# Kernel tuning notes

Measured on AMD Instinct MI355X. Metric: run time of the kernel, lower is better.

## Reference

```python
import jax, jax.numpy as jnp
import numpy as np
import math

S = 30.0
M = 0.5
COS_M = math.cos(M)
SIN_M = math.sin(M)
TH = math.cos(math.pi - M)  # threshold cos(pi - m)
EPS = 1e-12  # matches F.normalize default eps


def setup_inputs() -> dict:
    key = jax.random.key(0)
    k1, k2, k3 = jax.random.split(key, 3)
    B, D, C = 1024, 512, 100000
    inp = jax.random.normal(k1, (B, D), dtype=jnp.float32)
    label = jax.random.randint(k2, (B,), 0, C)
    # xavier_uniform_ for weight of shape (C, D): bound = sqrt(6/(C+D))
    bound = math.sqrt(6.0 / (C + D))
    weight = jax.random.uniform(k3, (C, D), dtype=jnp.float32, minval=-bound, maxval=bound)
    return {"input": inp, "label": label, "weight": weight}


def _l2norm(x):
    # F.normalize: x / max(||x||, eps)
    n = jnp.sqrt(jnp.sum(x * x, axis=-1, keepdims=True))
    return x / jnp.maximum(n, EPS)


def reference(input, label, weight):
    # cosine: [B, C]
    cosine = jnp.einsum('bd,cd->bc', _l2norm(input), _l2norm(weight))
    sine = jnp.sqrt(jnp.clip(1.0 - cosine * cosine, 0.0, 1.0))
    phi = cosine * COS_M - sine * SIN_M
    phi = jnp.where(cosine > TH, phi, cosine - S * SIN_M * M)
    # one-hot combine done via direct label-indexed select (avoids materializing one_hot)
    B, C = cosine.shape
    is_target = jnp.arange(C)[None, :] == label[:, None]  # [B, C] bool
    output = jnp.where(is_target, phi, cosine) * S
    return output
```

## Files before the change

### kernel.cpp

```cpp
#include <hip/hip_runtime.h>


#define MDIM 1024
#define KDIM 512
#define NCLS 100000

#define BM 128
#define BN 128
#define BK 32
#define LDST 40

#define NTILES ((NCLS + BN - 1) / BN)
#define NWG (8 * NTILES)

typedef unsigned short u16;
typedef unsigned int u32;
typedef short s16x8 __attribute__((ext_vector_type(8)));
typedef float f32x4 __attribute__((ext_vector_type(4)));

__device__ __forceinline__ u32 pk2(float a, float b) {
  u32 ua = __builtin_bit_cast(u32, a);
  u32 ub = __builtin_bit_cast(u32, b);
  ua += 0x7FFFu + ((ua >> 16) & 1u);
  ub += 0x7FFFu + ((ub >> 16) & 1u);
  return (ua >> 16) | (ub & 0xFFFF0000u);
}

__global__ __launch_bounds__(256) void norm_input_kernel(const float* __restrict__ in,
                                                         u16* __restrict__ abf) {
  const int row = blockIdx.x;
  const int tid = threadIdx.x;
  const float2 v = *reinterpret_cast<const float2*>(in + (size_t)row * KDIM + 2 * tid);
  float ss = v.x * v.x + v.y * v.y;
#pragma unroll
  for (int off = 32; off > 0; off >>= 1) ss += __shfl_down(ss, off);
  __shared__ float part[4];
  if ((tid & 63) == 0) part[tid >> 6] = ss;
  __syncthreads();
  const float tot = part[0] + part[1] + part[2] + part[3];
  const float rn = 1.0f / fmaxf(sqrtf(tot), 1e-12f);
  reinterpret_cast<u32*>(abf)[row * (KDIM / 2) + tid] = pk2(v.x * rn, v.y * rn);
}

__global__ __launch_bounds__(256) void norm_weight_kernel(const float* __restrict__ W,
                                                          u16* __restrict__ wbf) {
  const int row = blockIdx.x * 4 + (threadIdx.x >> 6);
  const int lane = threadIdx.x & 63;
  const float* p = W + (size_t)row * KDIM + lane * 8;
  const float4 v0 = *reinterpret_cast<const float4*>(p);
  const float4 v1 = *reinterpret_cast<const float4*>(p + 4);
  float ss = v0.x * v0.x + v0.y * v0.y + v0.z * v0.z + v0.w * v0.w
           + v1.x * v1.x + v1.y * v1.y + v1.z * v1.z + v1.w * v1.w;
#pragma unroll
  for (int off = 32; off > 0; off >>= 1) ss += __shfl_xor(ss, off);
  const float rn = 1.0f / fmaxf(sqrtf(ss), 1e-12f);
  uint4 o;
  o.x = pk2(v0.x * rn, v0.y * rn);
  o.y = pk2(v0.z * rn, v0.w * rn);
  o.z = pk2(v1.x * rn, v1.y * rn);
  o.w = pk2(v1.z * rn, v1.w * rn);
  *reinterpret_cast<uint4*>(wbf + (size_t)row * KDIM + lane * 8) = o;
}

__global__ __launch_bounds__(256) void arcface_gemm_bf16(const u16* __restrict__ Abf,
                                                         const u16* __restrict__ Wbf,
                                                         const int* __restrict__ label,
                                                         float* __restrict__ out) {
  __shared__ u16 lA[BM * LDST];
  __shared__ u16 lW[BN * LDST];
  __shared__ int lbl[BM];

  const int tid = threadIdx.x;
  const int orig = blockIdx.x;
  const int wg = (orig & 7) * NTILES + (orig >> 3);
  const int m0 = (wg & 7) * BM;
  const int n0 = (wg >> 3) * BN;

  if (tid < BM) lbl[tid] = label[m0 + tid];

  const int r = tid >> 1;
  const int half = tid & 1;
  int c = n0 + r;
  if (c >= NCLS) c = NCLS - 1;

  const u16* aptr = Abf + (size_t)(m0 + r) * KDIM + half * 16;
  const u16* wptr = Wbf + (size_t)c * KDIM + half * 16;

  uint4 a0 = *(const uint4*)(aptr);
  uint4 a1 = *(const uint4*)(aptr + 8);
  uint4 b0 = *(const uint4*)(wptr);
  uint4 b1 = *(const uint4*)(wptr + 8);

  f32x4 acc[4][4] = {};

  const int lane = tid & 63;
  const int wv = tid >> 6;
  const int wm = (wv & 1) * 64;
  const int wn = (wv >> 1) * 64;
  const int ln = lane & 15;
  const int kq = lane >> 4;

  const int aw = r * LDST + half * 16;

  for (int kt = 0; kt < KDIM / BK; ++kt) {
    __syncthreads();
    *(uint4*)&lA[aw] = a0;
    *(uint4*)&lA[aw + 8] = a1;
    *(uint4*)&lW[aw] = b0;
    *(uint4*)&lW[aw + 8] = b1;
    __syncthreads();

    if (kt < KDIM / BK - 1) {
      const u16* ap = aptr + (kt + 1) * BK;
      a0 = *(const uint4*)(ap);
      a1 = *(const uint4*)(ap + 8);
      const u16* wp = wptr + (kt + 1) * BK;
      b0 = *(const uint4*)(wp);
      b1 = *(const uint4*)(wp + 8);
    }

    s16x8 af[4], wf[4];
#pragma unroll
    for (int i = 0; i < 4; ++i)
      af[i] = *(const s16x8*)&lA[(wm + 16 * i + ln) * LDST + kq * 8];
#pragma unroll
    for (int j = 0; j < 4; ++j)
      wf[j] = *(const s16x8*)&lW[(wn + 16 * j + ln) * LDST + kq * 8];
#pragma unroll
    for (int i = 0; i < 4; ++i)
#pragma unroll
      for (int j = 0; j < 4; ++j)
        acc[i][j] = __builtin_amdgcn_mfma_f32_16x16x32_bf16(af[i], wf[j], acc[i][j], 0, 0, 0);
  }

  constexpr float S_ = 30.0f;
  constexpr float COS_M = 0.87758256189037276f;
  constexpr float SIN_M = 0.47942553860420301f;
  constexpr float TH_ = -0.87758256189037276f;
  constexpr float FALLB = 30.0f * 0.47942553860420301f * 0.5f;

#pragma unroll
  for (int i = 0; i < 4; ++i) {
    const int lrow_b = wm + 16 * i + 4 * kq;
#pragma unroll
    for (int j = 0; j < 4; ++j) {
      const int col = wn + 16 * j + ln;
      const int gcol = n0 + col;
      if (gcol < NCLS) {
#pragma unroll
        for (int rg = 0; rg < 4; ++rg) {
          const int lrow = lrow_b + rg;
          const float cosv = acc[i][j][rg];
          float o = S_ * cosv;
          if (gcol == lbl[lrow]) {
            const float s2 = fmaxf(1.0f - cosv * cosv, 0.0f);
            const float sine = sqrtf(s2);
            float phi = cosv * COS_M - sine * SIN_M;
            phi = (cosv > TH_) ? phi : (cosv - FALLB);
            o = S_ * phi;
          }
          __builtin_nontemporal_store(o, &out[(size_t)(m0 + lrow) * NCLS + gcol]);
        }
      }
    }
  }
}

__global__ __launch_bounds__(256) void arcface_gemm(const u16* __restrict__ Abf,
                                                    const float* __restrict__ W,
                                                    const int* __restrict__ label,
                                                    float* __restrict__ out) {
  __shared__ u16 lA[BM * LDST];
  __shared__ u16 lW[BN * LDST];
  __shared__ float rnw[BN];
  __shared__ int lbl[BM];

  const int tid = threadIdx.x;
  const int m0 = blockIdx.x * BM;
  const int n0 = blockIdx.y * BN;

  if (tid < BM) lbl[tid] = label[m0 + tid];

  const int r = tid >> 1;
  const int half = tid & 1;
  int c = n0 + r;
  if (c >= NCLS) c = NCLS - 1;

  const u16* aptr = Abf + (size_t)(m0 + r) * KDIM + half * 16;
  const float* wptr = W + (size_t)c * KDIM + half * 16;

  uint4 a0 = *(const uint4*)(aptr);
  uint4 a1 = *(const uint4*)(aptr + 8);
  float4 w0 = *(const float4*)(wptr);
  float4 w1 = *(const float4*)(wptr + 4);
  float4 w2 = *(const float4*)(wptr + 8);
  float4 w3 = *(const float4*)(wptr + 12);

  f32x4 acc[4][4] = {};
  float ss = 0.0f;

  const int lane = tid & 63;
  const int wv = tid >> 6;
  const int wm = (wv & 1) * 64;
  const int wn = (wv >> 1) * 64;
  const int ln = lane & 15;
  const int kq = lane >> 4;

  const int aw = r * LDST + half * 16;

  for (int kt = 0; kt < KDIM / BK; ++kt) {
    __syncthreads();
    *(uint4*)&lA[aw] = a0;
    *(uint4*)&lA[aw + 8] = a1;
    ss += w0.x * w0.x + w0.y * w0.y + w0.z * w0.z + w0.w * w0.w;
    ss += w1.x * w1.x + w1.y * w1.y + w1.z * w1.z + w1.w * w1.w;
    ss += w2.x * w2.x + w2.y * w2.y + w2.z * w2.z + w2.w * w2.w;
    ss += w3.x * w3.x + w3.y * w3.y + w3.z * w3.z + w3.w * w3.w;
    uint4 p0, p1;
    p0.x = pk2(w0.x, w0.y); p0.y = pk2(w0.z, w0.w);
    p0.z = pk2(w1.x, w1.y); p0.w = pk2(w1.z, w1.w);
    p1.x = pk2(w2.x, w2.y); p1.y = pk2(w2.z, w2.w);
    p1.z = pk2(w3.x, w3.y); p1.w = pk2(w3.z, w3.w);
    *(uint4*)&lW[aw] = p0;
    *(uint4*)&lW[aw + 8] = p1;
    __syncthreads();

    if (kt < KDIM / BK - 1) {
      const u16* ap = aptr + (kt + 1) * BK;
      a0 = *(const uint4*)(ap);
      a1 = *(const uint4*)(ap + 8);
      const float* wp = wptr + (kt + 1) * BK;
      w0 = *(const float4*)(wp);
      w1 = *(const float4*)(wp + 4);
      w2 = *(const float4*)(wp + 8);
      w3 = *(const float4*)(wp + 12);
    }

    s16x8 af[4], wf[4];
#pragma unroll
    for (int i = 0; i < 4; ++i)
      af[i] = *(const s16x8*)&lA[(wm + 16 * i + ln) * LDST + kq * 8];
#pragma unroll
    for (int j = 0; j < 4; ++j)
      wf[j] = *(const s16x8*)&lW[(wn + 16 * j + ln) * LDST + kq * 8];
#pragma unroll
    for (int i = 0; i < 4; ++i)
#pragma unroll
      for (int j = 0; j < 4; ++j)
        acc[i][j] = __builtin_amdgcn_mfma_f32_16x16x32_bf16(af[i], wf[j], acc[i][j], 0, 0, 0);
  }

  const float sst = ss + __shfl_xor(ss, 1);
  if (half == 0) rnw[r] = 1.0f / fmaxf(sqrtf(sst), 1e-12f);
  __syncthreads();

  constexpr float S_ = 30.0f;
  constexpr float COS_M = 0.87758256189037276f;
  constexpr float SIN_M = 0.47942553860420301f;
  constexpr float TH_ = -0.87758256189037276f;
  constexpr float FALLB = 30.0f * 0.47942553860420301f * 0.5f;

#pragma unroll
  for (int i = 0; i < 4; ++i) {
    const int lrow_b = wm + 16 * i + 4 * kq;
#pragma unroll
    for (int j = 0; j < 4; ++j) {
      const int col = wn + 16 * j + ln;
      const int gcol = n0 + col;
      const float rw = rnw[col];
      if (gcol < NCLS) {
#pragma unroll
        for (int rg = 0; rg < 4; ++rg) {
          const int lrow = lrow_b + rg;
          const float cosv = acc[i][j][rg] * rw;
          float o = S_ * cosv;
          if (gcol == lbl[lrow]) {
            const float s2 = fmaxf(1.0f - cosv * cosv, 0.0f);
            const float sine = sqrtf(s2);
            float phi = cosv * COS_M - sine * SIN_M;
            phi = (cosv > TH_) ? phi : (cosv - FALLB);
            o = S_ * phi;
          }
          out[(size_t)(m0 + lrow) * NCLS + gcol] = o;
        }
      }
    }
  }
}

extern "C" void kernel_launch(void* const* d_in, const int* in_sizes, int n_in,
                              void* d_out, int out_size, void* d_ws, size_t ws_size,
                              hipStream_t stream) {
  const float* input = (const float*)d_in[0];
  const int* label = (const int*)d_in[1];
  const float* weight = (const float*)d_in[2];
  float* out = (float*)d_out;
  u16* abf = (u16*)d_ws;

  hipLaunchKernelGGL(norm_input_kernel, dim3(MDIM), dim3(256), 0, stream, input, abf);

  const size_t a_bytes = (size_t)MDIM * KDIM * sizeof(u16);
  const size_t w_bytes = (size_t)NCLS * KDIM * sizeof(u16);
  if (ws_size >= a_bytes + w_bytes) {
    u16* wbf = abf + (size_t)MDIM * KDIM;
    hipLaunchKernelGGL(norm_weight_kernel, dim3(NCLS / 4), dim3(256), 0, stream, weight, wbf);
    hipLaunchKernelGGL(arcface_gemm_bf16, dim3(NWG), dim3(256), 0, stream, abf, wbf, label, out);
  } else {
    dim3 grid(MDIM / BM, (NCLS + BN - 1) / BN);
    hipLaunchKernelGGL(arcface_gemm, grid, dim3(256), 0, stream, abf, weight, label, out);
  }
}
```

Measured before the change: 719.2 us.

## Load GEMM tiles directly into LDS with global_load_lds and drop nontemporal stores

Replaces the register-staged global→LDS copy in the bf16 GEMM with direct global_load_lds DMA into a swizzled LDS layout matching MFMA fragment order. Fragments are read into registers before the next tile's async load is issued, which frees VGPRs and removes the explicit LDS write step. The output store also changes from nontemporal to a regular store. This relies on correct waitcnt handling between async LDS loads and the barrier, and the output is write-bound (400MB) so the gain may be limited.

Measured after the change: 785.1 us. 9.2% more time.

```diff
diff --git a/kernel.cpp b/kernel.cpp
--- a/kernel.cpp
+++ b/kernel.cpp
@@ -24,6 +24,12 @@
   ua += 0x7FFFu + ((ua >> 16) & 1u);
   ub += 0x7FFFu + ((ub >> 16) & 1u);
   return (ua >> 16) | (ub & 0xFFFF0000u);
+}
+
+__device__ __forceinline__ void gl16(const u16* g, u16* l) {
+  __builtin_amdgcn_global_load_lds(
+      (const __attribute__((address_space(1))) void*)g,
+      (__attribute__((address_space(3))) void*)l, 16, 0, 0);
 }
 
 __global__ __launch_bounds__(256) void norm_input_kernel(const float* __restrict__ in,
@@ -66,8 +72,8 @@
                                                          const u16* __restrict__ Wbf,
                                                          const int* __restrict__ label,
                                                          float* __restrict__ out) {
-  __shared__ u16 lA[BM * LDST];
-  __shared__ u16 lW[BN * LDST];
+  __shared__ u16 lA[BM * BK];
+  __shared__ u16 lW[BN * BK];
   __shared__ int lbl[BM];
 
   const int tid = threadIdx.x;
@@ -78,54 +84,52 @@
 
   if (tid < BM) lbl[tid] = label[m0 + tid];
 
-  const int r = tid >> 1;
-  const int half = tid & 1;
-  int c = n0 + r;
-  if (c >= NCLS) c = NCLS - 1;
-
-  const u16* aptr = Abf + (size_t)(m0 + r) * KDIM + half * 16;
-  const u16* wptr = Wbf + (size_t)c * KDIM + half * 16;
-
-  uint4 a0 = *(const uint4*)(aptr);
-  uint4 a1 = *(const uint4*)(aptr + 8);
-  uint4 b0 = *(const uint4*)(wptr);
-  uint4 b1 = *(const uint4*)(wptr + 8);
-
-  f32x4 acc[4][4] = {};
-
   const int lane = tid & 63;
   const int wv = tid >> 6;
+
+  const int sr = lane & 15;
+  const int sc = (lane >> 4) * 8;
+  const u16* aG0 = Abf + (size_t)(m0 + 16 * wv + sr) * KDIM + sc;
+  const u16* aG1 = aG0 + (size_t)64 * KDIM;
+  int wr0 = n0 + 16 * wv + sr;       if (wr0 >= NCLS) wr0 = NCLS - 1;
+  int wr1 = n0 + 64 + 16 * wv + sr;  if (wr1 >= NCLS) wr1 = NCLS - 1;
+  const u16* wG0 = Wbf + (size_t)wr0 * KDIM + sc;
+  const u16* wG1 = Wbf + (size_t)wr1 * KDIM + sc;
+  u16* const lA0 = &lA[wv * 512];
+  u16* const lA1 = &lA[(4 + wv) * 512];
+  u16* const lW0 = &lW[wv * 512];
+  u16* const lW1 = &lW[(4 + wv) * 512];
+
+  f32x4 acc[4][4] = {};
+
   const int wm = (wv & 1) * 64;
   const int wn = (wv >> 1) * 64;
   const int ln = lane & 15;
   const int kq = lane >> 4;
-
-  const int aw = r * LDST + half * 16;
+  const int sA = wm >> 4;
+  const int sW = wn >> 4;
+
+  gl16(aG0, lA0); gl16(aG1, lA1); gl16(wG0, lW0); gl16(wG1, lW1);
 
   for (int kt = 0; kt < KDIM / BK; ++kt) {
     __syncthreads();
-    *(uint4*)&lA[aw] = a0;
-    *(uint4*)&lA[aw + 8] = a1;
-    *(uint4*)&lW[aw] = b0;
-    *(uint4*)&lW[aw + 8] = b1;
+
+    s16x8 af[4], wf[4];
+#pragma unroll
+    for (int i = 0; i < 4; ++i)
+      af[i] = *(const s16x8*)&lA[(sA + i) * 512 + kq * 128 + ln * 8];
+#pragma unroll
+    for (int j = 0; j < 4; ++j)
+      wf[j] = *(const s16x8*)&lW[(sW + j) * 512 + kq * 128 + ln * 8];
+
     __syncthreads();
 
     if (kt < KDIM / BK - 1) {
-      const u16* ap = aptr + (kt + 1) * BK;
-      a0 = *(const uint4*)(ap);
-      a1 = *(const uint4*)(ap + 8);
-      const u16* wp = wptr + (kt + 1) * BK;
-      b0 = *(const uint4*)(wp);
-      b1 = *(const uint4*)(wp + 8);
+      const int o = (kt + 1) * BK;
+      gl16(aG0 + o, lA0); gl16(aG1 + o, lA1);
+      gl16(wG0 + o, lW0); gl16(wG1 + o, lW1);
     }
 
-    s16x8 af[4], wf[4];
-#pragma unroll
-    for (int i = 0; i < 4; ++i)
-      af[i] = *(const s16x8*)&lA[(wm + 16 * i + ln) * LDST + kq * 8];
-#pragma unroll
-    for (int j = 0; j < 4; ++j)
-      wf[j] = *(const s16x8*)&lW[(wn + 16 * j + ln) * LDST + kq * 8];
 #pragma unroll
     for (int i = 0; i < 4; ++i)
 #pragma unroll
@@ -159,7 +163,7 @@
             phi = (cosv > TH_) ? phi : (cosv - FALLB);
             o = S_ * phi;
           }
-          __builtin_nontemporal_store(o, &out[(size_t)(m0 + lrow) * NCLS + gcol]);
+          out[(size_t)(m0 + lrow) * NCLS + gcol] = o;
         }
       }
     }
```

## Load MFMA fragments directly from global memory, drop LDS staging and barriers

Applied to the files above, without the earlier changes.

The bf16 GEMM kernel no longer stages A and W tiles through shared memory with two barriers per k-step. Each lane now loads its MFMA fragments straight from global memory, relying on cache for reuse across waves, with the k-loop fully unrolled and launch bounds raised to request 3 blocks per CU. The epilogue reads labels from global memory per row and replaces nontemporal stores with ordinary stores. The trade is fewer barriers and LDS traffic against redundant global/L2 loads (each fragment is fetched by several waves) and possible cache pollution from the 400MB output.

Result: slower. 932.8 us (+29.7%).

```diff
diff --git a/kernel.cpp b/kernel.cpp
--- a/kernel.cpp
+++ b/kernel.cpp
@@ -62,36 +62,15 @@
   *reinterpret_cast<uint4*>(wbf + (size_t)row * KDIM + lane * 8) = o;
 }
 
-__global__ __launch_bounds__(256) void arcface_gemm_bf16(const u16* __restrict__ Abf,
-                                                         const u16* __restrict__ Wbf,
-                                                         const int* __restrict__ label,
-                                                         float* __restrict__ out) {
-  __shared__ u16 lA[BM * LDST];
-  __shared__ u16 lW[BN * LDST];
-  __shared__ int lbl[BM];
-
+__global__ __launch_bounds__(256, 3) void arcface_gemm_bf16(const u16* __restrict__ Abf,
+                                                            const u16* __restrict__ Wbf,
+                                                            const int* __restrict__ label,
+                                                            float* __restrict__ out) {
   const int tid = threadIdx.x;
   const int orig = blockIdx.x;
   const int wg = (orig & 7) * NTILES + (orig >> 3);
   const int m0 = (wg & 7) * BM;
   const int n0 = (wg >> 3) * BN;
-
-  if (tid < BM) lbl[tid] = label[m0 + tid];
-
-  const int r = tid >> 1;
-  const int half = tid & 1;
-  int c = n0 + r;
-  if (c >= NCLS) c = NCLS - 1;
-
-  const u16* aptr = Abf + (size_t)(m0 + r) * KDIM + half * 16;
-  const u16* wptr = Wbf + (size_t)c * KDIM + half * 16;
-
-  uint4 a0 = *(const uint4*)(aptr);
-  uint4 a1 = *(const uint4*)(aptr + 8);
-  uint4 b0 = *(const uint4*)(wptr);
-  uint4 b1 = *(const uint4*)(wptr + 8);
-
-  f32x4 acc[4][4] = {};
 
   const int lane = tid & 63;
   const int wv = tid >> 6;
@@ -100,32 +79,29 @@
   const int ln = lane & 15;
   const int kq = lane >> 4;
 
-  const int aw = r * LDST + half * 16;
-
+  const u16* ap[4];
+  const u16* wp[4];
+#pragma unroll
+  for (int i = 0; i < 4; ++i)
+    ap[i] = Abf + (size_t)(m0 + wm + 16 * i + ln) * KDIM + kq * 8;
+#pragma unroll
+  for (int j = 0; j < 4; ++j) {
+    int wrow = n0 + wn + 16 * j + ln;
+    if (wrow >= NCLS) wrow = NCLS - 1;
+    wp[j] = Wbf + (size_t)wrow * KDIM + kq * 8;
+  }
+
+  f32x4 acc[4][4] = {};
+
+#pragma unroll
   for (int kt = 0; kt < KDIM / BK; ++kt) {
-    __syncthreads();
-    *(uint4*)&lA[aw] = a0;
-    *(uint4*)&lA[aw + 8] = a1;
-    *(uint4*)&lW[aw] = b0;
-    *(uint4*)&lW[aw + 8] = b1;
-    __syncthreads();
-
-    if (kt < KDIM / BK - 1) {
-      const u16* ap = aptr + (kt + 1) * BK;
-      a0 = *(const uint4*)(ap);
-      a1 = *(const uint4*)(ap + 8);
-      const u16* wp = wptr + (kt + 1) * BK;
-      b0 = *(const uint4*)(wp);
-      b1 = *(const uint4*)(wp + 8);
-    }
-
     s16x8 af[4], wf[4];
 #pragma unroll
     for (int i = 0; i < 4; ++i)
-      af[i] = *(const s16x8*)&lA[(wm + 16 * i + ln) * LDST + kq * 8];
+      af[i] = *(const s16x8*)(ap[i] + kt * BK);
 #pragma unroll
     for (int j = 0; j < 4; ++j)
-      wf[j] = *(const s16x8*)&lW[(wn + 16 * j + ln) * LDST + kq * 8];
+      wf[j] = *(const s16x8*)(wp[j] + kt * BK);
 #pragma unroll
     for (int i = 0; i < 4; ++i)
 #pragma unroll
@@ -141,25 +117,25 @@
 
 #pragma unroll
   for (int i = 0; i < 4; ++i) {
-    const int lrow_b = wm + 16 * i + 4 * kq;
-#pragma unroll
-    for (int j = 0; j < 4; ++j) {
-      const int col = wn + 16 * j + ln;
-      const int gcol = n0 + col;
-      if (gcol < NCLS) {
-#pragma unroll
-        for (int rg = 0; rg < 4; ++rg) {
-          const int lrow = lrow_b + rg;
+#pragma unroll
+    for (int rg = 0; rg < 4; ++rg) {
+      const int lrow = wm + 16 * i + 4 * kq + rg;
+      const int row_lbl = label[m0 + lrow];
+      float* const orow = out + (size_t)(m0 + lrow) * NCLS;
+#pragma unroll
+      for (int j = 0; j < 4; ++j) {
+        const int gcol = n0 + wn + 16 * j + ln;
+        if (gcol < NCLS) {
           const float cosv = acc[i][j][rg];
           float o = S_ * cosv;
-          if (gcol == lbl[lrow]) {
+          if (gcol == row_lbl) {
             const float s2 = fmaxf(1.0f - cosv * cosv, 0.0f);
             const float sine = sqrtf(s2);
             float phi = cosv * COS_M - sine * SIN_M;
             phi = (cosv > TH_) ? phi : (cosv - FALLB);
             o = S_ * phi;
           }
-          __builtin_nontemporal_store(o, &out[(size_t)(m0 + lrow) * NCLS + gcol]);
+          orow[gcol] = o;
         }
       }
     }
```
